# Kernel tuning notes

Measured on AMD Instinct MI355X. Metric: run time of the kernel, lower is better.

The kernel has to match this reference:

```python
import jax, jax.numpy as jnp
import numpy as np

N = 100000  # nodes


def _gcn_conv(x, W, b, src, dst, dis, n):
    # GCNConv: linear transform first (out_dim small), then normalized aggregate
    h = x @ W                                   # [N, out]
    norm = dis[src] * dis[dst]                  # [E']
    msg = norm[:, None] * h[src]                # [E', out]
    out = jax.ops.segment_sum(msg, dst, num_segments=n)
    return out + b


def setup_inputs() -> dict:
    key = jax.random.key(0)
    ks = jax.random.split(key, 4)
    F_IN, HID, C, E = 512, 16, 16, 3200000
    x = jax.random.normal(ks[0], (N, F_IN), dtype=jnp.float32)
    edge_index = jax.random.randint(ks[1], (2, E), 0, N, dtype=jnp.int32)
    W1 = jax.random.normal(ks[2], (F_IN, HID), dtype=jnp.float32) * (1.0 / np.sqrt(F_IN))
    b1 = jnp.zeros((HID,), dtype=jnp.float32)
    W2 = jax.random.normal(ks[3], (HID, C), dtype=jnp.float32) * (1.0 / np.sqrt(HID))
    b2 = jnp.zeros((C,), dtype=jnp.float32)
    return {"x": x, "edge_index": edge_index, "W1": W1, "b1": b1, "W2": W2, "b2": b2}


def reference(x, edge_index, W1, b1, W2, b2):
    n = x.shape[0]
    loop = jnp.arange(n, dtype=edge_index.dtype)
    src = jnp.concatenate([edge_index[0], loop])  # add self-loops (GCNConv default)
    dst = jnp.concatenate([edge_index[1], loop])
    deg = jax.ops.segment_sum(jnp.ones_like(dst, dtype=x.dtype), dst, num_segments=n)
    dis = jnp.where(deg > 0, jax.lax.rsqrt(deg), 0.0)  # deg^{-1/2}
    # dropout is identity in eval mode
    h = jax.nn.elu(_gcn_conv(x, W1, b1, src, dst, dis, n))
    out = _gcn_conv(h, W2, b2, src, dst, dis, n)
    return jax.nn.log_softmax(out, axis=1)
```

## Files before the change

kernel.cpp:

```cpp
#include <hip/hip_runtime.h>

#define TPB 256
#define BKT_SHIFT 8
#define BKT_SZ 256
#define CHUNK 8192

__global__ void k_count(const int* __restrict__ dst, int* __restrict__ counts,
                        int E, int NB, int NCHUNK) {
  __shared__ int hist[512];
  int t = threadIdx.x;
  for (int d = t; d < NB; d += TPB) hist[d] = 0;
  __syncthreads();
  int base = blockIdx.x * CHUNK;
  for (int i = t; i < CHUNK; i += TPB) {
    int e = base + i;
    if (e < E) atomicAdd(&hist[dst[e] >> BKT_SHIFT], 1);
  }
  __syncthreads();
  for (int d = t; d < NB; d += TPB)
    counts[d * NCHUNK + blockIdx.x] = hist[d];
}

__global__ void k_scan1(int* __restrict__ a, int* __restrict__ btot, int total) {
  __shared__ int s[TPB];
  int t = threadIdx.x;
  int i = blockIdx.x * TPB + t;
  int v = (i < total) ? a[i] : 0;
  s[t] = v;
  __syncthreads();
  for (int d = 1; d < TPB; d <<= 1) {
    int u = (t >= d) ? s[t - d] : 0;
    __syncthreads();
    s[t] += u;
    __syncthreads();
  }
  if (i < total) a[i] = s[t] - v;
  if (t == TPB - 1) btot[blockIdx.x] = s[t];
}

__global__ void k_scan2(int* __restrict__ btot, int nb) {
  __shared__ int s[1024];
  int t = threadIdx.x;
  int v = (t < nb) ? btot[t] : 0;
  s[t] = v;
  __syncthreads();
  for (int d = 1; d < 1024; d <<= 1) {
    int u = (t >= d) ? s[t - d] : 0;
    __syncthreads();
    s[t] += u;
    __syncthreads();
  }
  if (t < nb) btot[t] = s[t] - v;
}

__global__ void k_scan3(int* __restrict__ a, const int* __restrict__ btot, int total) {
  int i = blockIdx.x * TPB + threadIdx.x;
  if (i < total) a[i] += btot[blockIdx.x];
}

__global__ void k_part(const int* __restrict__ src, const int* __restrict__ dst,
                       const int* __restrict__ bases, unsigned int* __restrict__ part,
                       int E, int NB, int NCHUNK) {
  __shared__ int cur[512];
  int t = threadIdx.x;
  for (int d = t; d < NB; d += TPB) cur[d] = bases[d * NCHUNK + blockIdx.x];
  __syncthreads();
  int base = blockIdx.x * CHUNK;
  for (int i = t; i < CHUNK; i += TPB) {
    int e = base + i;
    if (e < E) {
      int dv = dst[e];
      int d = dv >> BKT_SHIFT;
      int p = atomicAdd(&cur[d], 1);
      part[p] = ((unsigned)src[e] << BKT_SHIFT) | (unsigned)(dv & (BKT_SZ - 1));
    }
  }
}

__global__ __launch_bounds__(256) void k_build(
    const unsigned int* __restrict__ part, const int* __restrict__ bases,
    int* __restrict__ offs, int* __restrict__ csr, float* __restrict__ dis,
    int n, int E, int NB, int NCHUNK) {
  __shared__ int cnt[BKT_SZ];
  __shared__ int scn[BKT_SZ];
  int b = blockIdx.x, t = threadIdx.x;
  cnt[t] = 0;
  __syncthreads();
  int beg = bases[b * NCHUNK];
  int end = (b + 1 < NB) ? bases[(b + 1) * NCHUNK] : E;
  for (int e = beg + t; e < end; e += 256)
    atomicAdd(&cnt[part[e] & (BKT_SZ - 1)], 1);
  __syncthreads();
  int deg = cnt[t];
  scn[t] = deg;
  __syncthreads();
  for (int d = 1; d < 256; d <<= 1) {
    int u = (t >= d) ? scn[t - d] : 0;
    __syncthreads();
    scn[t] += u;
    __syncthreads();
  }
  int excl = scn[t] - deg;
  int node = b * BKT_SZ + t;
  if (node < n) {
    offs[node] = beg + excl;
    dis[node] = 1.0f / sqrtf((float)(deg + 1));
  }
  if (b == NB - 1 && t == 0) offs[n] = E;
  __syncthreads();
  cnt[t] = beg + excl;
  __syncthreads();
  for (int e = beg + t; e < end; e += 256) {
    unsigned int en = part[e];
    int p = atomicAdd(&cnt[en & (BKT_SZ - 1)], 1);
    csr[p] = (int)(en >> BKT_SHIFT);
  }
}

__global__ __launch_bounds__(256) void k_gemm1(
    const float* __restrict__ x, const float* __restrict__ W1,
    const float* __restrict__ dis, float* __restrict__ hs, int n, int nwaves) {
  const int lane = threadIdx.x & 63;
  const int wave = blockIdx.x * 4 + (threadIdx.x >> 6);

  float w[8][16];
  #pragma unroll
  for (int m = 0; m < 8; ++m) {
    #pragma unroll
    for (int q = 0; q < 4; ++q) {
      float4 t = *reinterpret_cast<const float4*>(W1 + (lane * 8 + m) * 16 + q * 4);
      w[m][q * 4 + 0] = t.x; w[m][q * 4 + 1] = t.y;
      w[m][q * 4 + 2] = t.z; w[m][q * 4 + 3] = t.w;
    }
  }
  const int c_out = ((lane & 1) << 3) | ((lane & 2) << 1) | ((lane & 4) >> 1) | ((lane & 8) >> 3);

  for (int i = wave; i < n; i += nwaves) {
    const float4* xp = reinterpret_cast<const float4*>(x + (size_t)i * 512);
    float4 a = xp[lane * 2], b = xp[lane * 2 + 1];
    float xv[8] = {a.x, a.y, a.z, a.w, b.x, b.y, b.z, b.w};

    float acc[16];
    #pragma unroll
    for (int c = 0; c < 16; ++c) acc[c] = 0.f;
    #pragma unroll
    for (int m = 0; m < 8; ++m) {
      #pragma unroll
      for (int c = 0; c < 16; ++c) acc[c] = fmaf(xv[m], w[m][c], acc[c]);
    }

    {
      const bool hi = (lane & 1) != 0;
      #pragma unroll
      for (int v = 0; v < 8; ++v) {
        float send = hi ? acc[v] : acc[v + 8];
        float rcv = __shfl_xor(send, 1);
        acc[v] = (hi ? acc[v + 8] : acc[v]) + rcv;
      }
    }
    {
      const bool hi = (lane & 2) != 0;
      #pragma unroll
      for (int v = 0; v < 4; ++v) {
        float send = hi ? acc[v] : acc[v + 4];
        float rcv = __shfl_xor(send, 2);
        acc[v] = (hi ? acc[v + 4] : acc[v]) + rcv;
      }
    }
    {
      const bool hi = (lane & 4) != 0;
      #pragma unroll
      for (int v = 0; v < 2; ++v) {
        float send = hi ? acc[v] : acc[v + 2];
        float rcv = __shfl_xor(send, 4);
        acc[v] = (hi ? acc[v + 2] : acc[v]) + rcv;
      }
    }
    {
      const bool hi = (lane & 8) != 0;
      float send = hi ? acc[0] : acc[1];
      float rcv = __shfl_xor(send, 8);
      acc[0] = (hi ? acc[1] : acc[0]) + rcv;
    }
    float vsum = acc[0];
    vsum += __shfl_xor(vsum, 16);
    vsum += __shfl_xor(vsum, 32);

    if (lane < 16) hs[(size_t)i * 16 + c_out] = dis[i] * vsum;
  }
}

__global__ __launch_bounds__(256) void k_agg1(
    const int* __restrict__ offs, const int* __restrict__ csr,
    const float* __restrict__ hs, const float* __restrict__ dis,
    const float* __restrict__ b1, float* __restrict__ h1s, int n) {
  int wave = blockIdx.x * 4 + (threadIdx.x >> 6);
  if (wave >= n) return;
  int lane = threadIdx.x & 63;
  int c = lane & 15, r = lane >> 4;
  int beg = offs[wave], end = offs[wave + 1];
  float acc = 0.f;
  #pragma unroll 2
  for (int k = beg + r; k < end; k += 4)
    acc += hs[(size_t)csr[k] * 16 + c];
  acc += __shfl_xor(acc, 16);
  acc += __shfl_xor(acc, 32);
  acc += hs[(size_t)wave * 16 + c];
  float di = dis[wave];
  float o = fmaf(di, acc, b1[c]);
  float h1 = o > 0.f ? o : expm1f(o);
  if (r == 0) h1s[(size_t)wave * 16 + c] = di * h1;
}

__global__ __launch_bounds__(256) void k_agg2(
    const int* __restrict__ offs, const int* __restrict__ csr,
    const float* __restrict__ h1s, const float* __restrict__ dis,
    const float* __restrict__ W2, const float* __restrict__ b2,
    float* __restrict__ out, int n) {
  __shared__ float w2s[256];
  w2s[threadIdx.x] = W2[threadIdx.x];
  __syncthreads();
  int wave = blockIdx.x * 4 + (threadIdx.x >> 6);
  if (wave >= n) return;
  int lane = threadIdx.x & 63;
  int c = lane & 15, r = lane >> 4;
  int beg = offs[wave], end = offs[wave + 1];
  float acc = 0.f;
  #pragma unroll 2
  for (int k = beg + r; k < end; k += 4)
    acc += h1s[(size_t)csr[k] * 16 + c];
  acc += __shfl_xor(acc, 16);
  acc += __shfl_xor(acc, 32);
  acc += h1s[(size_t)wave * 16 + c];
  float di = dis[wave];
  float dot = 0.f;
  #pragma unroll
  for (int k = 0; k < 16; ++k) {
    float vk = __shfl(acc, k, 16);
    dot = fmaf(di * vk, w2s[k * 16 + c], dot);
  }
  float o = dot + b2[c];
  float m = o;
  m = fmaxf(m, __shfl_xor(m, 1));
  m = fmaxf(m, __shfl_xor(m, 2));
  m = fmaxf(m, __shfl_xor(m, 4));
  m = fmaxf(m, __shfl_xor(m, 8));
  float ex = expf(o - m);
  float ssum = ex;
  ssum += __shfl_xor(ssum, 1);
  ssum += __shfl_xor(ssum, 2);
  ssum += __shfl_xor(ssum, 4);
  ssum += __shfl_xor(ssum, 8);
  if (r == 0) out[(size_t)wave * 16 + c] = o - m - logf(ssum);
}

extern "C" void kernel_launch(void* const* d_in, const int* in_sizes, int n_in,
                              void* d_out, int out_size, void* d_ws, size_t ws_size,
                              hipStream_t stream) {
  const float* x  = (const float*)d_in[0];
  const int*   ei = (const int*)d_in[1];
  const float* W1 = (const float*)d_in[2];
  const float* b1 = (const float*)d_in[3];
  const float* W2 = (const float*)d_in[4];
  const float* b2 = (const float*)d_in[5];
  float* out = (float*)d_out;

  const int n = in_sizes[0] / 512;
  const int E = in_sizes[1] / 2;
  const int* src = ei;
  const int* dst = ei + E;

  const int NB = (n + BKT_SZ - 1) >> BKT_SHIFT;
  const int NCHUNK = (E + CHUNK - 1) / CHUNK;
  const int total = NB * NCHUNK;
  const int sb = (total + TPB - 1) / TPB;

  char* ws = (char*)d_ws;
  size_t off = 0;
  auto alloc = [&](size_t bytes) -> void* {
    void* p = (void*)(ws + off);
    off += (bytes + 255) & ~(size_t)255;
    return p;
  };
  int*          counts = (int*)alloc((size_t)total * 4);
  int*          btot   = (int*)alloc(1024 * 4);
  unsigned int* part   = (unsigned int*)alloc((size_t)E * 4);
  int*          offs   = (int*)alloc((size_t)(n + 1) * 4);
  int*          csr    = (int*)alloc((size_t)E * 4);
  float*        dis    = (float*)alloc((size_t)n * 4);
  float*        hs     = (float*)alloc((size_t)n * 16 * 4);
  float*        h1s    = (float*)alloc((size_t)n * 16 * 4);
  (void)ws_size; (void)n_in; (void)out_size;

  const int ab = (n + 3) / 4;

  k_count<<<NCHUNK, TPB, 0, stream>>>(dst, counts, E, NB, NCHUNK);
  k_scan1<<<sb, TPB, 0, stream>>>(counts, btot, total);
  k_scan2<<<1, 1024, 0, stream>>>(btot, sb);
  k_scan3<<<sb, TPB, 0, stream>>>(counts, btot, total);
  k_part <<<NCHUNK, TPB, 0, stream>>>(src, dst, counts, part, E, NB, NCHUNK);
  k_build<<<NB, TPB, 0, stream>>>(part, counts, offs, csr, dis, n, E, NB, NCHUNK);
  k_gemm1<<<2048, TPB, 0, stream>>>(x, W1, dis, hs, n, 2048 * 4);
  k_agg1 <<<ab, TPB, 0, stream>>>(offs, csr, hs, dis, b1, h1s, n);
  k_agg2 <<<ab, TPB, 0, stream>>>(offs, csr, h1s, dis, W2, b2, out, n);
}
```

Measured before the change: 558.5 us.

## Fold scan fixup into consumers, vectorize aggregation gathers, prefetch GEMM rows

Removes the k_scan3 launch by having k_part and k_build add the block offset from btot when they read the counts. Rewrites both aggregation kernels so each lane gathers a float4 (4 lanes per neighbor row, 16 neighbors in flight per wave) with the next csr index prefetched, replacing scalar 16-lane gathers that covered 4 neighbors at a time. Adds software prefetch of the next x row in k_gemm1. This raises memory-level parallelism for the gathers at the cost of more registers and more shuffles in the reductions and the W2 product.

```diff
diff --git a/kernel.cpp b/kernel.cpp
--- a/kernel.cpp
+++ b/kernel.cpp
@@ -53,17 +53,15 @@
   if (t < nb) btot[t] = s[t] - v;
 }
 
-__global__ void k_scan3(int* __restrict__ a, const int* __restrict__ btot, int total) {
-  int i = blockIdx.x * TPB + threadIdx.x;
-  if (i < total) a[i] += btot[blockIdx.x];
-}
-
 __global__ void k_part(const int* __restrict__ src, const int* __restrict__ dst,
-                       const int* __restrict__ bases, unsigned int* __restrict__ part,
-                       int E, int NB, int NCHUNK) {
+                       const int* __restrict__ cnts, const int* __restrict__ btot,
+                       unsigned int* __restrict__ part, int E, int NB, int NCHUNK) {
   __shared__ int cur[512];
   int t = threadIdx.x;
-  for (int d = t; d < NB; d += TPB) cur[d] = bases[d * NCHUNK + blockIdx.x];
+  for (int d = t; d < NB; d += TPB) {
+    int idx = d * NCHUNK + blockIdx.x;
+    cur[d] = cnts[idx] + btot[idx >> 8];
+  }
   __syncthreads();
   int base = blockIdx.x * CHUNK;
   for (int i = t; i < CHUNK; i += TPB) {
@@ -78,7 +76,8 @@
 }
 
 __global__ __launch_bounds__(256) void k_build(
-    const unsigned int* __restrict__ part, const int* __restrict__ bases,
+    const unsigned int* __restrict__ part, const int* __restrict__ cnts,
+    const int* __restrict__ btot,
     int* __restrict__ offs, int* __restrict__ csr, float* __restrict__ dis,
     int n, int E, int NB, int NCHUNK) {
   __shared__ int cnt[BKT_SZ];
@@ -86,8 +85,13 @@
   int b = blockIdx.x, t = threadIdx.x;
   cnt[t] = 0;
   __syncthreads();
-  int beg = bases[b * NCHUNK];
-  int end = (b + 1 < NB) ? bases[(b + 1) * NCHUNK] : E;
+  int i0 = b * NCHUNK;
+  int beg = cnts[i0] + btot[i0 >> 8];
+  int end = E;
+  if (b + 1 < NB) {
+    int i1 = (b + 1) * NCHUNK;
+    end = cnts[i1] + btot[i1 >> 8];
+  }
   for (int e = beg + t; e < end; e += 256)
     atomicAdd(&cnt[part[e] & (BKT_SZ - 1)], 1);
   __syncthreads();
@@ -135,11 +139,21 @@
   }
   const int c_out = ((lane & 1) << 3) | ((lane & 2) << 1) | ((lane & 4) >> 1) | ((lane & 8) >> 3);
 
-  for (int i = wave; i < n; i += nwaves) {
-    const float4* xp = reinterpret_cast<const float4*>(x + (size_t)i * 512);
-    float4 a = xp[lane * 2], b = xp[lane * 2 + 1];
+  float4 a = {0, 0, 0, 0}, b = {0, 0, 0, 0};
+  if (wave < n) {
+    const float4* xp = reinterpret_cast<const float4*>(x + (size_t)wave * 512);
+    a = xp[lane * 2]; b = xp[lane * 2 + 1];
+  }
+
+  for (int i = wave; i < n; ) {
+    int inext = i + nwaves;
+    float4 an = {0, 0, 0, 0}, bn = {0, 0, 0, 0};
+    if (inext < n) {
+      const float4* xp = reinterpret_cast<const float4*>(x + (size_t)inext * 512);
+      an = xp[lane * 2]; bn = xp[lane * 2 + 1];
+    }
+
     float xv[8] = {a.x, a.y, a.z, a.w, b.x, b.y, b.z, b.w};
-
     float acc[16];
     #pragma unroll
     for (int c = 0; c < 16; ++c) acc[c] = 0.f;
@@ -187,6 +201,8 @@
     vsum += __shfl_xor(vsum, 32);
 
     if (lane < 16) hs[(size_t)i * 16 + c_out] = dis[i] * vsum;
+
+    a = an; b = bn; i = inext;
   }
 }
 
@@ -197,19 +213,38 @@
   int wave = blockIdx.x * 4 + (threadIdx.x >> 6);
   if (wave >= n) return;
   int lane = threadIdx.x & 63;
-  int c = lane & 15, r = lane >> 4;
+  int c4 = lane & 3, r = lane >> 2;
   int beg = offs[wave], end = offs[wave + 1];
-  float acc = 0.f;
-  #pragma unroll 2
-  for (int k = beg + r; k < end; k += 4)
-    acc += hs[(size_t)csr[k] * 16 + c];
-  acc += __shfl_xor(acc, 16);
-  acc += __shfl_xor(acc, 32);
-  acc += hs[(size_t)wave * 16 + c];
+  const float4* hs4 = reinterpret_cast<const float4*>(hs);
+
+  float ax = 0.f, ay = 0.f, az = 0.f, aw = 0.f;
+  int k = beg + r;
+  int s = (k < end) ? csr[k] : 0;
+  while (k < end) {
+    int k2 = k + 16;
+    int s2 = (k2 < end) ? csr[k2] : 0;
+    float4 v = hs4[(size_t)s * 4 + c4];
+    ax += v.x; ay += v.y; az += v.z; aw += v.w;
+    s = s2; k = k2;
+  }
+  #pragma unroll
+  for (int m = 4; m <= 32; m <<= 1) {
+    ax += __shfl_xor(ax, m); ay += __shfl_xor(ay, m);
+    az += __shfl_xor(az, m); aw += __shfl_xor(aw, m);
+  }
+  float4 sf = hs4[(size_t)wave * 4 + c4];
   float di = dis[wave];
-  float o = fmaf(di, acc, b1[c]);
-  float h1 = o > 0.f ? o : expm1f(o);
-  if (r == 0) h1s[(size_t)wave * 16 + c] = di * h1;
+  float4 b1v = reinterpret_cast<const float4*>(b1)[c4];
+  float ox = fmaf(di, ax + sf.x, b1v.x);
+  float oy = fmaf(di, ay + sf.y, b1v.y);
+  float oz = fmaf(di, az + sf.z, b1v.z);
+  float ow = fmaf(di, aw + sf.w, b1v.w);
+  float4 o;
+  o.x = di * (ox > 0.f ? ox : expm1f(ox));
+  o.y = di * (oy > 0.f ? oy : expm1f(oy));
+  o.z = di * (oz > 0.f ? oz : expm1f(oz));
+  o.w = di * (ow > 0.f ? ow : expm1f(ow));
+  if (r == 0) reinterpret_cast<float4*>(h1s)[(size_t)wave * 4 + c4] = o;
 }
 
 __global__ __launch_bounds__(256) void k_agg2(
@@ -223,21 +258,40 @@
   int wave = blockIdx.x * 4 + (threadIdx.x >> 6);
   if (wave >= n) return;
   int lane = threadIdx.x & 63;
-  int c = lane & 15, r = lane >> 4;
+  int c4 = lane & 3, r = lane >> 2;
   int beg = offs[wave], end = offs[wave + 1];
-  float acc = 0.f;
-  #pragma unroll 2
-  for (int k = beg + r; k < end; k += 4)
-    acc += h1s[(size_t)csr[k] * 16 + c];
-  acc += __shfl_xor(acc, 16);
-  acc += __shfl_xor(acc, 32);
-  acc += h1s[(size_t)wave * 16 + c];
+  const float4* h4 = reinterpret_cast<const float4*>(h1s);
+
+  float ax = 0.f, ay = 0.f, az = 0.f, aw = 0.f;
+  int k = beg + r;
+  int s = (k < end) ? csr[k] : 0;
+  while (k < end) {
+    int k2 = k + 16;
+    int s2 = (k2 < end) ? csr[k2] : 0;
+    float4 v = h4[(size_t)s * 4 + c4];
+    ax += v.x; ay += v.y; az += v.z; aw += v.w;
+    s = s2; k = k2;
+  }
+  #pragma unroll
+  for (int m = 4; m <= 32; m <<= 1) {
+    ax += __shfl_xor(ax, m); ay += __shfl_xor(ay, m);
+    az += __shfl_xor(az, m); aw += __shfl_xor(aw, m);
+  }
+  float4 sf = h4[(size_t)wave * 4 + c4];
   float di = dis[wave];
+  float sx = di * (ax + sf.x);
+  float sy = di * (ay + sf.y);
+  float sz = di * (az + sf.z);
+  float sw = di * (aw + sf.w);
+  int c = lane & 15;
+  int lbase = lane & ~3;
   float dot = 0.f;
   #pragma unroll
-  for (int k = 0; k < 16; ++k) {
-    float vk = __shfl(acc, k, 16);
-    dot = fmaf(di * vk, w2s[k * 16 + c], dot);
+  for (int k16 = 0; k16 < 16; ++k16) {
+    int srcl = lbase | (k16 >> 2);
+    float comp = (k16 & 3) == 0 ? sx : (k16 & 3) == 1 ? sy : (k16 & 3) == 2 ? sz : sw;
+    float vk = __shfl(comp, srcl);
+    dot = fmaf(vk, w2s[k16 * 16 + c], dot);
   }
   float o = dot + b2[c];
   float m = o;
@@ -251,7 +305,7 @@
   ssum += __shfl_xor(ssum, 2);
   ssum += __shfl_xor(ssum, 4);
   ssum += __shfl_xor(ssum, 8);
-  if (r == 0) out[(size_t)wave * 16 + c] = o - m - logf(ssum);
+  if (lane < 16) out[(size_t)wave * 16 + c] = o - m - logf(ssum);
 }
 
 extern "C" void kernel_launch(void* const* d_in, const int* in_sizes, int n_in,
@@ -297,9 +351,8 @@
   k_count<<<NCHUNK, TPB, 0, stream>>>(dst, counts, E, NB, NCHUNK);
   k_scan1<<<sb, TPB, 0, stream>>>(counts, btot, total);
   k_scan2<<<1, 1024, 0, stream>>>(btot, sb);
-  k_scan3<<<sb, TPB, 0, stream>>>(counts, btot, total);
-  k_part <<<NCHUNK, TPB, 0, stream>>>(src, dst, counts, part, E, NB, NCHUNK);
-  k_build<<<NB, TPB, 0, stream>>>(part, counts, offs, csr, dis, n, E, NB, NCHUNK);
+  k_part <<<NCHUNK, TPB, 0, stream>>>(src, dst, counts, btot, part, E, NB, NCHUNK);
+  k_build<<<NB, TPB, 0, stream>>>(part, counts, btot, offs, csr, dis, n, E, NB, NCHUNK);
   k_gemm1<<<2048, TPB, 0, stream>>>(x, W1, dis, hs, n, 2048 * 4);
   k_agg1 <<<ab, TPB, 0, stream>>>(offs, csr, hs, dis, b1, h1s, n);
   k_agg2 <<<ab, TPB, 0, stream>>>(offs, csr, h1s, dis, W2, b2, out, n);
```

New measurement: 543.8 us. 2.6% less time.
